# Optimization experiments

Hardware: AMD Instinct MI355X
Metric: run time of the kernel (lower is better)

## Reference

```python
import jax, jax.numpy as jnp
import numpy as np

N = 200000          # active voxels
C = 128             # channels (in == out, required by final elementwise multiply)
GRID = (256, 256, 64)
EPS = 1e-5


def setup_inputs() -> dict:
    rng = np.random.default_rng(0)
    total = GRID[0] * GRID[1] * GRID[2]
    lin = rng.choice(total, size=N, replace=False)
    coords = np.stack(np.unravel_index(lin, GRID), axis=1).astype(np.int64)  # [N,3]
    # dense voxel -> row lookup table; sentinel N means 'no active voxel here'
    lut = np.full(total, N, dtype=np.int32)
    lut[lin] = np.arange(N, dtype=np.int32)
    nb = np.full((3, 2, N), N, dtype=np.int32)  # [axis, {prev,next}, N]
    hi = np.array(GRID) - 1
    for a in range(3):
        for s, off in enumerate((-1, 1)):
            c = coords.copy()
            c[:, a] += off
            valid = (c[:, a] >= 0) & (c[:, a] <= hi[a])
            cc = np.clip(c, 0, hi)
            lin_n = np.ravel_multi_index(tuple(cc.T), GRID)
            nb[a, s] = np.where(valid, lut[lin_n], N)
    kf, kw, kg, kb = jax.random.split(jax.random.key(0), 4)
    features = jax.random.normal(kf, (N, C), jnp.float32)
    W = jax.random.normal(kw, (3, 3, C, C), jnp.float32) * (1.0 / np.sqrt(3.0 * C))
    gamma = 1.0 + 0.1 * jax.random.normal(kg, (3, C), jnp.float32)
    beta = 0.1 * jax.random.normal(kb, (3, C), jnp.float32)
    return {"features": features, "nb_idx": jnp.asarray(nb), "W": W,
            "gamma": gamma, "beta": beta}


def reference(features, nb_idx, W, gamma, beta):
    # zero pad row: gathering sentinel index N yields a zero contribution
    xp = jnp.concatenate([features, jnp.zeros((1, C), features.dtype)], axis=0)
    acc = jnp.zeros_like(features)
    for a in range(3):  # three 1D decomposition axes (3x1x1, 1x3x1, 1x1x3)
        prev = xp[nb_idx[a, 0]]                      # [N,C]
        nxt = xp[nb_idx[a, 1]]                       # [N,C]
        out = prev @ W[a, 0] + features @ W[a, 1] + nxt @ W[a, 2]
        # BatchNorm1d (training-mode batch stats, biased variance)
        mu = out.mean(axis=0)
        var = out.var(axis=0)
        out = (out - mu) * jax.lax.rsqrt(var + EPS) * gamma[a] + beta[a]
        acc = acc + jax.nn.sigmoid(out)
    return acc * features
```

## Files before the change

### kernel.cpp

```cpp
#include <hip/hip_runtime.h>
#include <hip/hip_bf16.h>

#define NVOX 200000
#define CCH  128
#define KTOT 384
#define EPS_BN 1e-5f
#define PB   625
#define TPB  5

typedef __bf16 bf16x8 __attribute__((ext_vector_type(8)));
typedef float  floatx4 __attribute__((ext_vector_type(4)));

#define XBF_OFF    0ull
#define XBF_BYTES  ((size_t)(NVOX + 1) * CCH * 2)
#define WT_OFF     (XBF_OFF + XBF_BYTES)
#define WT_BYTES   ((size_t)3 * CCH * KTOT * 2)
#define OUTB_OFF   (WT_OFF + WT_BYTES)
#define OUTB_BYTES ((size_t)3 * NVOX * CCH * 2)
#define STATS_OFF  (OUTB_OFF + OUTB_BYTES)
#define STATS_BYTES ((size_t)3 * 2 * CCH * 4)

__global__ void k_prep_x(const float* __restrict__ xf, __bf16* __restrict__ xbf) {
    int idx = blockIdx.x * blockDim.x + threadIdx.x;
    const int total = (NVOX + 1) * 16;
    if (idx >= total) return;
    float v[8];
    if (idx < NVOX * 16) {
        const float4* p = (const float4*)xf + (size_t)idx * 2;
        float4 f0 = p[0], f1 = p[1];
        v[0] = f0.x; v[1] = f0.y; v[2] = f0.z; v[3] = f0.w;
        v[4] = f1.x; v[5] = f1.y; v[6] = f1.z; v[7] = f1.w;
    } else {
        #pragma unroll
        for (int j = 0; j < 8; ++j) v[j] = 0.0f;
    }
    bf16x8 o;
    #pragma unroll
    for (int j = 0; j < 8; ++j) o[j] = (__bf16)v[j];
    *((bf16x8*)xbf + idx) = o;
}

__global__ void k_prep_w(const float* __restrict__ W, __bf16* __restrict__ wt) {
    int idx = blockIdx.x * blockDim.x + threadIdx.x;
    if (idx >= 3 * CCH * KTOT) return;
    int k = idx % KTOT; int rem = idx / KTOT;
    int c = rem % CCH;  int a = rem / CCH;
    int s = k >> 7, k0 = k & 127;
    wt[idx] = (__bf16)W[(((size_t)(a * 3 + s) * CCH) + k0) * CCH + c];
}

__launch_bounds__(256, 2)
__global__ void k_gemm(const __bf16* __restrict__ xbf, const __bf16* __restrict__ wt,
                       const int* __restrict__ nb, __bf16* __restrict__ outb,
                       float* __restrict__ stats) {
    __shared__ __align__(16) __bf16 smemA[64 * 384];
    __shared__ __align__(16) __bf16 smemO[64 * 136];
    __shared__ int s_pn[2][128];

    const int a    = blockIdx.y;
    const int tid  = threadIdx.x;
    const int w    = tid >> 6;
    const int lane = tid & 63;
    const int q    = lane >> 4;
    const int ln   = lane & 15;
    const int e    = ln & 7;

    const __bf16* wbase = wt + (size_t)a * CCH * KTOT;
    bf16x8 B0[12], B1[12];
    #pragma unroll
    for (int ks = 0; ks < 12; ++ks) {
        B0[ks] = *(const bf16x8*)(wbase + (size_t)(w * 32 + ln) * KTOT + ks * 32 + q * 8);
        B1[ks] = *(const bf16x8*)(wbase + (size_t)(w * 32 + 16 + ln) * KTOT + ks * 32 + q * 8);
    }

    float s0 = 0.f, ss0 = 0.f, s1 = 0.f, ss1 = 0.f;

    int r_pn = 0;
    if (tid < 128) {
        const size_t nbase = (size_t)(a * 2 + (tid >> 6)) * NVOX + (tid & 63);
        r_pn = nb[nbase + blockIdx.x * 64];
        s_pn[0][tid] = r_pn;
        r_pn = nb[nbase + (blockIdx.x + PB) * 64];
    }
    __syncthreads();

    for (int ti = 0; ti < TPB; ++ti) {
        const int row0 = (blockIdx.x + ti * PB) * 64;
        const int buf  = ti & 1;

        #pragma unroll
        for (int it = 0; it < 12; ++it) {
            int p    = it * 256 + tid;
            int r    = p / 48;
            int spos = p - r * 48;
            int slog = spos ^ (r & 7);
            int src  = slog >> 4, ch = slog & 15;
            int g    = (src == 1) ? (row0 + r) : s_pn[buf][(src >> 1) * 64 + r];
            const __bf16* gp = xbf + (size_t)g * CCH + ch * 8;
            __builtin_amdgcn_global_load_lds(
                (const __attribute__((address_space(1))) void*)gp,
                (__attribute__((address_space(3))) void*)(&smemA[(it * 256 + w * 64) * 8]),
                16, 0, 0);
        }
        if (ti + 1 < TPB && tid < 128) s_pn[buf ^ 1][tid] = r_pn;
        __syncthreads();

        if (ti + 2 < TPB && tid < 128)
            r_pn = nb[(size_t)(a * 2 + (tid >> 6)) * NVOX
                      + (blockIdx.x + (ti + 2) * PB) * 64 + (tid & 63)];

        floatx4 acc0[4], acc1[4];
        #pragma unroll
        for (int mt = 0; mt < 4; ++mt)
            #pragma unroll
            for (int r = 0; r < 4; ++r) { acc0[mt][r] = 0.0f; acc1[mt][r] = 0.0f; }

        #pragma unroll
        for (int ks = 0; ks < 12; ++ks) {
            #pragma unroll
            for (int mt = 0; mt < 4; ++mt) {
                int rr = mt * 16 + ln;
                int sp = (ks * 4 + q) ^ e;
                bf16x8 afr = *(const bf16x8*)(&smemA[rr * 384 + sp * 8]);
                acc0[mt] = __builtin_amdgcn_mfma_f32_16x16x32_bf16(afr, B0[ks], acc0[mt], 0, 0, 0);
                acc1[mt] = __builtin_amdgcn_mfma_f32_16x16x32_bf16(afr, B1[ks], acc1[mt], 0, 0, 0);
            }
        }

        #pragma unroll
        for (int mt = 0; mt < 4; ++mt)
            #pragma unroll
            for (int r = 0; r < 4; ++r) {
                float v0 = acc0[mt][r]; s0 += v0; ss0 += v0 * v0;
                float v1 = acc1[mt][r]; s1 += v1; ss1 += v1 * v1;
            }

        #pragma unroll
        for (int mt = 0; mt < 4; ++mt) {
            #pragma unroll
            for (int r = 0; r < 4; ++r) {
                int rr = mt * 16 + q * 4 + r;
                smemO[rr * 136 + w * 32 + ln]      = (__bf16)acc0[mt][r];
                smemO[rr * 136 + w * 32 + 16 + ln] = (__bf16)acc1[mt][r];
            }
        }
        __syncthreads();

        #pragma unroll
        for (int it2 = 0; it2 < 4; ++it2) {
            int i = it2 * 256 + tid;
            int r = i >> 4, ch = i & 15;
            bf16x8 v = *(const bf16x8*)(&smemO[r * 136 + ch * 8]);
            *(bf16x8*)(outb + ((size_t)a * NVOX + row0 + r) * CCH + ch * 8) = v;
        }
    }

    s0 += __shfl_xor(s0, 16); ss0 += __shfl_xor(ss0, 16);
    s0 += __shfl_xor(s0, 32); ss0 += __shfl_xor(ss0, 32);
    s1 += __shfl_xor(s1, 16); ss1 += __shfl_xor(ss1, 16);
    s1 += __shfl_xor(s1, 32); ss1 += __shfl_xor(ss1, 32);
    if (lane < 16) {
        int c0 = w * 32 + lane, c1 = w * 32 + 16 + lane;
        atomicAdd(&stats[a * 2 * CCH + c0], s0);
        atomicAdd(&stats[a * 2 * CCH + CCH + c0], ss0);
        atomicAdd(&stats[a * 2 * CCH + c1], s1);
        atomicAdd(&stats[a * 2 * CCH + CCH + c1], ss1);
    }
}

__launch_bounds__(256)
__global__ void k_final(const __bf16* __restrict__ outb, const float* __restrict__ xf,
                        const float* __restrict__ stats, const float* __restrict__ gamma,
                        const float* __restrict__ beta, float* __restrict__ out) {
    __shared__ float lsc[384], lsh[384];
    int tid = threadIdx.x;
    for (int i = tid; i < 384; i += 256) {
        int a = i >> 7, c = i & 127;
        float mu  = stats[a * 256 + c] * (1.0f / NVOX);
        float var = stats[a * 256 + 128 + c] * (1.0f / NVOX) - mu * mu;
        float rs  = rsqrtf(var + EPS_BN);
        float g = gamma[i], b = beta[i];
        lsc[i] = rs * g;
        lsh[i] = b - mu * rs * g;
    }
    __syncthreads();
    const int total = NVOX * 16;
    for (int idx = blockIdx.x * 256 + tid; idx < total; idx += gridDim.x * 256) {
        int c0 = (idx & 15) * 8;
        float4 f0 = ((const float4*)xf)[(size_t)idx * 2];
        float4 f1 = ((const float4*)xf)[(size_t)idx * 2 + 1];
        float r[8];
        #pragma unroll
        for (int j = 0; j < 8; ++j) r[j] = 0.0f;
        #pragma unroll
        for (int a = 0; a < 3; ++a) {
            bf16x8 o = *((const bf16x8*)outb + (size_t)a * NVOX * 16 + idx);
            #pragma unroll
            for (int j = 0; j < 8; ++j) {
                float v = (float)o[j] * lsc[a * 128 + c0 + j] + lsh[a * 128 + c0 + j];
                r[j] += __builtin_amdgcn_rcpf(1.0f + __expf(-v));
            }
        }
        float4 o0, o1;
        o0.x = r[0] * f0.x; o0.y = r[1] * f0.y; o0.z = r[2] * f0.z; o0.w = r[3] * f0.w;
        o1.x = r[4] * f1.x; o1.y = r[5] * f1.y; o1.z = r[6] * f1.z; o1.w = r[7] * f1.w;
        ((float4*)out)[(size_t)idx * 2]     = o0;
        ((float4*)out)[(size_t)idx * 2 + 1] = o1;
    }
}

extern "C" void kernel_launch(void* const* d_in, const int* in_sizes, int n_in,
                              void* d_out, int out_size, void* d_ws, size_t ws_size,
                              hipStream_t stream) {
    const float* xf    = (const float*)d_in[0];
    const int*   nb    = (const int*)  d_in[1];
    const float* W     = (const float*)d_in[2];
    const float* gamma = (const float*)d_in[3];
    const float* beta  = (const float*)d_in[4];
    float* out = (float*)d_out;

    char* ws = (char*)d_ws;
    __bf16* xbf   = (__bf16*)(ws + XBF_OFF);
    __bf16* wt    = (__bf16*)(ws + WT_OFF);
    __bf16* outb  = (__bf16*)(ws + OUTB_OFF);
    float*  stats = (float*)(ws + STATS_OFF);

    hipMemsetAsync(stats, 0, STATS_BYTES, stream);
    k_prep_x<<<((NVOX + 1) * 16 + 255) / 256, 256, 0, stream>>>(xf, xbf);
    k_prep_w<<<(3 * CCH * KTOT + 255) / 256, 256, 0, stream>>>(W, wt);
    k_gemm<<<dim3(PB, 3), 256, 0, stream>>>(xbf, wt, nb, outb, stats);
    k_final<<<2048, 256, 0, stream>>>(outb, xf, stats, gamma, beta, out);
}
```

Before: 359.0 us.

## Skip empty-neighbor MFMA slices, store GEMM output in fragment layout, fuse prep kernels

Result: slower. 586.7 us (+63.4%).

```diff
diff --git a/kernel.cpp b/kernel.cpp
--- a/kernel.cpp
+++ b/kernel.cpp
@@ -7,8 +7,10 @@
 #define EPS_BN 1e-5f
 #define PB   625
 #define TPB  5
+#define NTILE 3125
 
 typedef __bf16 bf16x8 __attribute__((ext_vector_type(8)));
+typedef __bf16 bf16x4 __attribute__((ext_vector_type(4)));
 typedef float  floatx4 __attribute__((ext_vector_type(4)));
 
 #define XBF_OFF    0ull
@@ -20,42 +22,44 @@
 #define STATS_OFF  (OUTB_OFF + OUTB_BYTES)
 #define STATS_BYTES ((size_t)3 * 2 * CCH * 4)
 
-__global__ void k_prep_x(const float* __restrict__ xf, __bf16* __restrict__ xbf) {
+__global__ void k_prep(const float* __restrict__ xf, __bf16* __restrict__ xbf,
+                       const float* __restrict__ W, __bf16* __restrict__ wt,
+                       float* __restrict__ stats) {
     int idx = blockIdx.x * blockDim.x + threadIdx.x;
-    const int total = (NVOX + 1) * 16;
-    if (idx >= total) return;
-    float v[8];
-    if (idx < NVOX * 16) {
-        const float4* p = (const float4*)xf + (size_t)idx * 2;
-        float4 f0 = p[0], f1 = p[1];
-        v[0] = f0.x; v[1] = f0.y; v[2] = f0.z; v[3] = f0.w;
-        v[4] = f1.x; v[5] = f1.y; v[6] = f1.z; v[7] = f1.w;
-    } else {
-        #pragma unroll
-        for (int j = 0; j < 8; ++j) v[j] = 0.0f;
-    }
-    bf16x8 o;
-    #pragma unroll
-    for (int j = 0; j < 8; ++j) o[j] = (__bf16)v[j];
-    *((bf16x8*)xbf + idx) = o;
-}
-
-__global__ void k_prep_w(const float* __restrict__ W, __bf16* __restrict__ wt) {
-    int idx = blockIdx.x * blockDim.x + threadIdx.x;
-    if (idx >= 3 * CCH * KTOT) return;
-    int k = idx % KTOT; int rem = idx / KTOT;
-    int c = rem % CCH;  int a = rem / CCH;
-    int s = k >> 7, k0 = k & 127;
-    wt[idx] = (__bf16)W[(((size_t)(a * 3 + s) * CCH) + k0) * CCH + c];
-}
-
-__launch_bounds__(256, 2)
+    const int XC = (NVOX + 1) * 16;
+    if (idx < XC) {
+        float v[8];
+        if (idx < NVOX * 16) {
+            const float4* p = (const float4*)xf + (size_t)idx * 2;
+            float4 f0 = p[0], f1 = p[1];
+            v[0] = f0.x; v[1] = f0.y; v[2] = f0.z; v[3] = f0.w;
+            v[4] = f1.x; v[5] = f1.y; v[6] = f1.z; v[7] = f1.w;
+        } else {
+            #pragma unroll
+            for (int j = 0; j < 8; ++j) v[j] = 0.0f;
+        }
+        bf16x8 o;
+        #pragma unroll
+        for (int j = 0; j < 8; ++j) o[j] = (__bf16)v[j];
+        *((bf16x8*)xbf + idx) = o;
+    } else if (idx < XC + 3 * CCH * KTOT) {
+        int j = idx - XC;
+        int k = j % KTOT; int rem = j / KTOT;
+        int c = rem % CCH;  int a = rem / CCH;
+        int s = k >> 7, k0 = k & 127;
+        wt[j] = (__bf16)W[(((size_t)(a * 3 + s) * CCH) + k0) * CCH + c];
+    } else if (idx < XC + 3 * CCH * KTOT + 768) {
+        stats[idx - XC - 3 * CCH * KTOT] = 0.0f;
+    }
+}
+
+__launch_bounds__(256, 3)
 __global__ void k_gemm(const __bf16* __restrict__ xbf, const __bf16* __restrict__ wt,
                        const int* __restrict__ nb, __bf16* __restrict__ outb,
                        float* __restrict__ stats) {
     __shared__ __align__(16) __bf16 smemA[64 * 384];
-    __shared__ __align__(16) __bf16 smemO[64 * 136];
     __shared__ int s_pn[2][128];
+    __shared__ int s_msk[2][2];
 
     const int a    = blockIdx.y;
     const int tid  = threadIdx.x;
@@ -80,12 +84,25 @@
         const size_t nbase = (size_t)(a * 2 + (tid >> 6)) * NVOX + (tid & 63);
         r_pn = nb[nbase + blockIdx.x * 64];
         s_pn[0][tid] = r_pn;
-        r_pn = nb[nbase + (blockIdx.x + PB) * 64];
-    }
+    }
+    {
+        unsigned long long m = 0;
+        if (tid < 128) m = __ballot(r_pn == NVOX);
+        if (tid == 0 || tid == 64) {
+            int pm = 0;
+            #pragma unroll
+            for (int gg = 0; gg < 4; ++gg)
+                if (((m >> (gg * 16)) & 0xFFFFull) == 0xFFFFull) pm |= 1 << gg;
+            s_msk[0][tid >> 6] = pm;
+        }
+    }
+    if (tid < 128)
+        r_pn = nb[(size_t)(a * 2 + (tid >> 6)) * NVOX + (tid & 63) + (blockIdx.x + PB) * 64];
     __syncthreads();
 
     for (int ti = 0; ti < TPB; ++ti) {
-        const int row0 = (blockIdx.x + ti * PB) * 64;
+        const int tIdx = blockIdx.x + ti * PB;
+        const int row0 = tIdx * 64;
         const int buf  = ti & 1;
 
         #pragma unroll
@@ -102,13 +119,27 @@
                 (__attribute__((address_space(3))) void*)(&smemA[(it * 256 + w * 64) * 8]),
                 16, 0, 0);
         }
-        if (ti + 1 < TPB && tid < 128) s_pn[buf ^ 1][tid] = r_pn;
+        if (ti + 1 < TPB) {
+            if (tid < 128) s_pn[buf ^ 1][tid] = r_pn;
+            unsigned long long m = 0;
+            if (tid < 128) m = __ballot(r_pn == NVOX);
+            if (tid == 0 || tid == 64) {
+                int pm = 0;
+                #pragma unroll
+                for (int gg = 0; gg < 4; ++gg)
+                    if (((m >> (gg * 16)) & 0xFFFFull) == 0xFFFFull) pm |= 1 << gg;
+                s_msk[buf ^ 1][tid >> 6] = pm;
+            }
+        }
         __syncthreads();
 
         if (ti + 2 < TPB && tid < 128)
             r_pn = nb[(size_t)(a * 2 + (tid >> 6)) * NVOX
                       + (blockIdx.x + (ti + 2) * PB) * 64 + (tid & 63)];
 
+        const int pm = __builtin_amdgcn_readfirstlane(s_msk[buf][0]);
+        const int nm = __builtin_amdgcn_readfirstlane(s_msk[buf][1]);
+
         floatx4 acc0[4], acc1[4];
         #pragma unroll
         for (int mt = 0; mt < 4; ++mt)
@@ -116,14 +147,29 @@
             for (int r = 0; r < 4; ++r) { acc0[mt][r] = 0.0f; acc1[mt][r] = 0.0f; }
 
         #pragma unroll
-        for (int ks = 0; ks < 12; ++ks) {
-            #pragma unroll
-            for (int mt = 0; mt < 4; ++mt) {
-                int rr = mt * 16 + ln;
-                int sp = (ks * 4 + q) ^ e;
-                bf16x8 afr = *(const bf16x8*)(&smemA[rr * 384 + sp * 8]);
+        for (int mt = 0; mt < 4; ++mt) {
+            const int rr = mt * 16 + ln;
+            #pragma unroll
+            for (int ks = 4; ks < 8; ++ks) {
+                bf16x8 afr = *(const bf16x8*)(&smemA[rr * 384 + (((ks * 4 + q) ^ e) * 8)]);
                 acc0[mt] = __builtin_amdgcn_mfma_f32_16x16x32_bf16(afr, B0[ks], acc0[mt], 0, 0, 0);
                 acc1[mt] = __builtin_amdgcn_mfma_f32_16x16x32_bf16(afr, B1[ks], acc1[mt], 0, 0, 0);
+            }
+            if (!((pm >> mt) & 1)) {
+                #pragma unroll
+                for (int ks = 0; ks < 4; ++ks) {
+                    bf16x8 afr = *(const bf16x8*)(&smemA[rr * 384 + (((ks * 4 + q) ^ e) * 8)]);
+                    acc0[mt] = __builtin_amdgcn_mfma_f32_16x16x32_bf16(afr, B0[ks], acc0[mt], 0, 0, 0);
+                    acc1[mt] = __builtin_amdgcn_mfma_f32_16x16x32_bf16(afr, B1[ks], acc1[mt], 0, 0, 0);
+                }
+            }
+            if (!((nm >> mt) & 1)) {
+                #pragma unroll
+                for (int ks = 8; ks < 12; ++ks) {
+                    bf16x8 afr = *(const bf16x8*)(&smemA[rr * 384 + (((ks * 4 + q) ^ e) * 8)]);
+                    acc0[mt] = __builtin_amdgcn_mfma_f32_16x16x32_bf16(afr, B0[ks], acc0[mt], 0, 0, 0);
+                    acc1[mt] = __builtin_amdgcn_mfma_f32_16x16x32_bf16(afr, B1[ks], acc1[mt], 0, 0, 0);
+                }
             }
         }
 
@@ -135,23 +181,18 @@
                 float v1 = acc1[mt][r]; s1 += v1; ss1 += v1 * v1;
             }
 
-        #pragma unroll
-        for (int mt = 0; mt < 4; ++mt) {
-            #pragma unroll
-            for (int r = 0; r < 4; ++r) {
-                int rr = mt * 16 + q * 4 + r;
-                smemO[rr * 136 + w * 32 + ln]      = (__bf16)acc0[mt][r];
-                smemO[rr * 136 + w * 32 + 16 + ln] = (__bf16)acc1[mt][r];
-            }
-        }
         __syncthreads();
 
-        #pragma unroll
-        for (int it2 = 0; it2 < 4; ++it2) {
-            int i = it2 * 256 + tid;
-            int r = i >> 4, ch = i & 15;
-            bf16x8 v = *(const bf16x8*)(&smemO[r * 136 + ch * 8]);
-            *(bf16x8*)(outb + ((size_t)a * NVOX + row0 + r) * CCH + ch * 8) = v;
+        {
+            __bf16* ob = outb + ((size_t)(a * NTILE + tIdx)) * 8192 + lane * 4;
+            #pragma unroll
+            for (int mt = 0; mt < 4; ++mt) {
+                bf16x4 v0, v1;
+                #pragma unroll
+                for (int r = 0; r < 4; ++r) { v0[r] = (__bf16)acc0[mt][r]; v1[r] = (__bf16)acc1[mt][r]; }
+                *(bf16x4*)(ob + ((w * 2 + 0) * 4 + mt) * 256) = v0;
+                *(bf16x4*)(ob + ((w * 2 + 1) * 4 + mt) * 256) = v1;
+            }
         }
     }
 
@@ -184,28 +225,32 @@
         lsh[i] = b - mu * rs * g;
     }
     __syncthreads();
-    const int total = NVOX * 16;
-    for (int idx = blockIdx.x * 256 + tid; idx < total; idx += gridDim.x * 256) {
-        int c0 = (idx & 15) * 8;
-        float4 f0 = ((const float4*)xf)[(size_t)idx * 2];
-        float4 f1 = ((const float4*)xf)[(size_t)idx * 2 + 1];
-        float r[8];
-        #pragma unroll
-        for (int j = 0; j < 8; ++j) r[j] = 0.0f;
+    const int total = NTILE * 2048;
+    for (int c = blockIdx.x * 256 + tid; c < total; c += gridDim.x * 256) {
+        int t     = c >> 11;
+        int cc    = c & 2047;
+        int g     = cc >> 6;
+        int lane2 = cc & 63;
+        int mt    = g & 3, h = g >> 2;
+        int qq    = lane2 >> 4, lnn = lane2 & 15;
+        int col   = h * 16 + lnn;
+        int row   = t * 64 + mt * 16 + qq * 4;
+        float r[4] = {0.f, 0.f, 0.f, 0.f};
         #pragma unroll
         for (int a = 0; a < 3; ++a) {
-            bf16x8 o = *((const bf16x8*)outb + (size_t)a * NVOX * 16 + idx);
-            #pragma unroll
-            for (int j = 0; j < 8; ++j) {
-                float v = (float)o[j] * lsc[a * 128 + c0 + j] + lsh[a * 128 + c0 + j];
+            bf16x4 o = *(const bf16x4*)(outb + ((size_t)(a * NTILE + t)) * 8192 + g * 256 + lane2 * 4);
+            float sc = lsc[a * 128 + col], sh = lsh[a * 128 + col];
+            #pragma unroll
+            for (int j = 0; j < 4; ++j) {
+                float v = (float)o[j] * sc + sh;
                 r[j] += __builtin_amdgcn_rcpf(1.0f + __expf(-v));
             }
         }
-        float4 o0, o1;
-        o0.x = r[0] * f0.x; o0.y = r[1] * f0.y; o0.z = r[2] * f0.z; o0.w = r[3] * f0.w;
-        o1.x = r[4] * f1.x; o1.y = r[5] * f1.y; o1.z = r[6] * f1.z; o1.w = r[7] * f1.w;
-        ((float4*)out)[(size_t)idx * 2]     = o0;
-        ((float4*)out)[(size_t)idx * 2 + 1] = o1;
+        #pragma unroll
+        for (int j = 0; j < 4; ++j) {
+            size_t off = (size_t)(row + j) * CCH + col;
+            out[off] = r[j] * xf[off];
+        }
     }
 }
 
@@ -225,9 +270,8 @@
     __bf16* outb  = (__bf16*)(ws + OUTB_OFF);
     float*  stats = (float*)(ws + STATS_OFF);
 
-    hipMemsetAsync(stats, 0, STATS_BYTES, stream);
-    k_prep_x<<<((NVOX + 1) * 16 + 255) / 256, 256, 0, stream>>>(xf, xbf);
-    k_prep_w<<<(3 * CCH * KTOT + 255) / 256, 256, 0, stream>>>(W, wt);
+    const int prep_items = (NVOX + 1) * 16 + 3 * CCH * KTOT + 768;
+    k_prep<<<(prep_items + 255) / 256, 256, 0, stream>>>(xf, xbf, W, wt, stats);
     k_gemm<<<dim3(PB, 3), 256, 0, stream>>>(xbf, wt, nb, outb, stats);
     k_final<<<2048, 256, 0, stream>>>(outb, xf, stats, gamma, beta, out);
 }
```
